# Kernel optimization log

Hardware: AMD Instinct MI355X
Metric: run time of the kernel (lower is better)

The kernel has to match this reference:

```python
import jax, jax.numpy as jnp
import numpy as np

N, E, B = 4096, 4096, 128  # nodes, edges, graphs


def _param(key, shape, scale):
    return jax.random.normal(key, shape, dtype=jnp.float32) * scale


def setup_inputs() -> dict:
    key = jax.random.key(0)
    ks = jax.random.split(key, 32)
    inp = {
        "x": jax.random.normal(ks[0], (N, 37), dtype=jnp.float32),
        "edge_index": jax.random.randint(ks[1], (2, E), 0, N),
        "edge_attr": jax.random.uniform(ks[2], (E, 5), dtype=jnp.float32),
        "batch": jnp.sort(jax.random.randint(ks[3], (N,), 0, B)),
        # NNConv 1: edge-MLP 5->512->37*128, root [37,128]
        "nn1_w1": _param(ks[4], (5, 512), 0.3),
        "nn1_b1": jnp.zeros((512,), jnp.float32),
        "nn1_w2": _param(ks[5], (512, 37 * 128), 0.01),
        "nn1_b2": jnp.zeros((37 * 128,), jnp.float32),
        "root1": _param(ks[6], (37, 128), 0.1),
        "bias1": jnp.zeros((128,), jnp.float32),
        # NNConv 2: edge-MLP 5->128->128*256, root [128,256]
        "nn2_w1": _param(ks[7], (5, 128), 0.3),
        "nn2_b1": jnp.zeros((128,), jnp.float32),
        "nn2_w2": _param(ks[8], (128, 128 * 256), 0.005),
        "nn2_b2": jnp.zeros((128 * 256,), jnp.float32),
        "root2": _param(ks[9], (128, 256), 0.05),
        "bias2": jnp.zeros((256,), jnp.float32),
        # NNConv 3: edge-MLP 5->128->256*256, root [256,256]
        "nn3_w1": _param(ks[10], (5, 128), 0.3),
        "nn3_b1": jnp.zeros((128,), jnp.float32),
        "nn3_w2": _param(ks[11], (128, 256 * 256), 0.005),
        "nn3_b2": jnp.zeros((256 * 256,), jnp.float32),
        "root3": _param(ks[12], (256, 256), 0.05),
        "bias3": jnp.zeros((256,), jnp.float32),
        # readout MLP
        "fc1_w": _param(ks[13], (256, 128), 0.06),
        "fc1_b": jnp.zeros((128,), jnp.float32),
        "fc2_w": _param(ks[14], (128, 64), 0.09),
        "fc2_b": jnp.zeros((64,), jnp.float32),
        "fc3_w": _param(ks[15], (64, 1), 0.12),
        "fc3_b": jnp.zeros((1,), jnp.float32),
    }
    return inp


def _nnconv(x, src, dst, edge_attr, w1, b1, w2, b2, root, bias, cin, cout):
    # edge MLP -> per-edge weight matrix [E, cin, cout]
    h = jax.nn.relu(edge_attr @ w1 + b1)
    W = (h @ w2 + b2).reshape(-1, cin, cout)
    # gather source features, per-edge matvec, scatter-add to targets
    msg = jnp.einsum('ei,eio->eo', x[src], W)          # [E, cout]
    agg = jax.ops.segment_sum(msg, dst, num_segments=x.shape[0])
    return agg + x @ root + bias


def _segment_mean(x, seg, num_segments):
    s = jax.ops.segment_sum(x, seg, num_segments=num_segments)
    cnt = jax.ops.segment_sum(jnp.ones((x.shape[0],), x.dtype), seg,
                              num_segments=num_segments)
    return s / jnp.maximum(cnt, 1.0)[:, None]


def reference(x, edge_index, edge_attr, batch,
              nn1_w1, nn1_b1, nn1_w2, nn1_b2, root1, bias1,
              nn2_w1, nn2_b1, nn2_w2, nn2_b2, root2, bias2,
              nn3_w1, nn3_b1, nn3_w2, nn3_b2, root3, bias3,
              fc1_w, fc1_b, fc2_w, fc2_b, fc3_w, fc3_b):
    src, dst = edge_index[0], edge_index[1]
    h = jax.nn.elu(_nnconv(x, src, dst, edge_attr, nn1_w1, nn1_b1, nn1_w2,
                           nn1_b2, root1, bias1, 37, 128))
    h = jax.nn.elu(_nnconv(h, src, dst, edge_attr, nn2_w1, nn2_b1, nn2_w2,
                           nn2_b2, root2, bias2, 128, 256))
    h = jax.nn.elu(_nnconv(h, src, dst, edge_attr, nn3_w1, nn3_b1, nn3_w2,
                           nn3_b2, root3, bias3, 256, 256))
    g = _segment_mean(h, batch, B)                     # [B, 256]
    g = jax.nn.elu(g @ fc1_w + fc1_b)
    g = jax.nn.elu(g @ fc2_w + fc2_b)
    g = g @ fc3_w + fc3_b
    return g.reshape(-1)
```

## Files before the change

kernel.cpp:

```cpp
#include <hip/hip_runtime.h>
#include <cstdint>
#include <cstddef>

typedef float f32x4 __attribute__((ext_vector_type(4)));
typedef _Float16 f16x8 __attribute__((ext_vector_type(8)));
typedef _Float16 f16x4 __attribute__((ext_vector_type(4)));

__device__ __forceinline__ float elu_f(float x) { return x > 0.f ? x : expm1f(x); }

__device__ __forceinline__ void gload_lds16(const void* g, void* l)
{
    __builtin_amdgcn_global_load_lds(
        (const __attribute__((address_space(1))) void*)g,
        (__attribute__((address_space(3))) void*)l,
        16, 0, 0);
}

__global__ __launch_bounds__(256)
void edge_mlp_kernel(const float* __restrict__ ea,
                     const int* __restrict__ dst, int* __restrict__ cnt,
                     const float* __restrict__ w1a, const float* __restrict__ b1a, _Float16* __restrict__ h1T,
                     const float* __restrict__ w1b, const float* __restrict__ b1b, _Float16* __restrict__ h2T,
                     const float* __restrict__ w1c, const float* __restrict__ b1c, _Float16* __restrict__ h3T,
                     int E)
{
    const int e0  = blockIdx.x * 64;
    const int tid = threadIdx.x;
    const int el  = tid & 63;
    const int cg  = tid >> 6;
    if (tid < 64) atomicAdd(&cnt[dst[e0 + tid]], 1);
    __shared__ float a[64][5];
    for (int i = tid; i < 320; i += 256) a[i / 5][i % 5] = ea[e0 * 5 + i];
    __syncthreads();
    float av[5];
    #pragma unroll
    for (int j = 0; j < 5; ++j) av[j] = a[el][j];

    #pragma unroll 4
    for (int t = 0; t < 128; ++t) {
        const int ch = t * 4 + cg;
        float s = b1a[ch];
        #pragma unroll
        for (int j = 0; j < 5; ++j) s = fmaf(av[j], w1a[j * 512 + ch], s);
        h1T[(size_t)ch * E + e0 + el] = (_Float16)fmaxf(s, 0.f);
    }
    #pragma unroll 4
    for (int t = 0; t < 32; ++t) {
        const int ch = t * 4 + cg;
        float s = b1b[ch];
        float u = b1c[ch];
        #pragma unroll
        for (int j = 0; j < 5; ++j) {
            s = fmaf(av[j], w1b[j * 128 + ch], s);
            u = fmaf(av[j], w1c[j * 128 + ch], u);
        }
        h2T[(size_t)ch * E + e0 + el] = (_Float16)fmaxf(s, 0.f);
        h3T[(size_t)ch * E + e0 + el] = (_Float16)fmaxf(u, 0.f);
    }
}

template <int CIN, int COUT, int KFTOT>
__global__ __launch_bounds__(256)
void pack_w2_kernel(const float* __restrict__ w2, const float* __restrict__ b2,
                    _Float16* __restrict__ w2h, int KH)
{
    __shared__ float tile[32][COUT + 2];
    const int bid = blockIdx.x;
    const int kh  = bid / KFTOT;
    const int c   = bid - kh * KFTOT;
    const int tid = threadIdx.x;
    const int CP  = 32 * COUT;
    for (int i = tid; i < CP; i += 256) {
        int kk = i / COUT, n = i - kk * COUT;
        int kg = c * 32 + kk;
        float v = 0.f;
        if (kg < CIN) v = (kh < KH) ? w2[((size_t)kh * CIN + kg) * COUT + n]
                                    : b2[(size_t)kg * COUT + n];
        tile[kk][n] = v;
    }
    __syncthreads();
    _Float16* outp = w2h + (size_t)bid * CP;
    for (int i = tid; i < CP; i += 256) {
        int n = i >> 5, kk = i & 31;
        int blk = (kk >> 3) ^ ((n >> 1) & 3);
        outp[n * 32 + blk * 8 + (kk & 7)] = (_Float16)tile[kk][n];
    }
}

__global__ __launch_bounds__(256)
void csr_scan_graph_kernel(const int* __restrict__ cnt, int* __restrict__ offs, int N,
                           const int* __restrict__ batch, int* __restrict__ goffs, int B,
                           int NN)
{
    __shared__ int sums[256];
    __shared__ int pref[257];
    const int tid = threadIdx.x;
    const int per = N / 256;
    int loc = 0;
    for (int i = 0; i < per; ++i) loc += cnt[tid * per + i];
    sums[tid] = loc;
    __syncthreads();
    if (tid == 0) {
        int s = 0; pref[0] = 0;
        for (int i = 0; i < 256; ++i) { s += sums[i]; pref[i + 1] = s; }
    }
    __syncthreads();
    int run = pref[tid];
    for (int i = 0; i < per; ++i) { offs[tid * per + i] = run; run += cnt[tid * per + i]; }
    if (tid == 255) offs[N] = run;
    for (int g = tid; g <= B; g += 256) {
        int lo = 0, hi = NN;
        while (lo < hi) { int mid = (lo + hi) >> 1; if (batch[mid] < g) lo = mid + 1; else hi = mid; }
        goffs[g] = lo;
    }
}

__global__ __launch_bounds__(256)
void csr_fill_kernel(const int* __restrict__ dst, const int* __restrict__ offs,
                     int* __restrict__ cur, int* __restrict__ eid, int E)
{
    int e = blockIdx.x * 256 + threadIdx.x;
    if (e < E) {
        int d = dst[e];
        int p = offs[d] + atomicAdd(&cur[d], 1);
        eid[p] = e;
    }
}

template <int KH, int CIN, int COUT, int KFTOT, int CSPLIT, int NY>
__global__ __launch_bounds__(256, 4)
void msg_mfma_kernel(const float* __restrict__ xin,
                     const _Float16* __restrict__ hT,
                     const _Float16* __restrict__ w2h,
                     const int* __restrict__ src,
                     _Float16* __restrict__ part,
                     int E, int khg_per)
{
    constexpr int BM = 128;
    constexpr int KF = KFTOT / CSPLIT;

    __shared__ __align__(16) _Float16 bsh[2][KF][64][32];
    __shared__ _Float16 s_h[2][BM];
    __shared__ int s_src[BM];

    const int tid  = threadIdx.x;
    const int lane = tid & 63;
    const int w    = tid >> 6;
    const int l15  = lane & 15;
    const int lg   = lane >> 4;
    const int swb  = (l15 >> 1) & 3;

    const int nwg = gridDim.x;
    const int bid = blockIdx.x;
    const int swz = (bid & 7) * (nwg >> 3) + (bid >> 3);
    const int m    = swz & 31;
    const int rest = swz >> 5;
    const int y    = rest % NY;
    const int zz   = rest / NY;
    const int cinH = zz % CSPLIT;
    const int zkh  = zz / CSPLIT;

    const int e0  = m * BM;
    const int n0  = y * 64;
    const int k0  = cinH * KF * 32;
    const int kh0 = zkh * khg_per;
    const int kh1 = min(kh0 + khg_per, KH + 1);

    if (tid < BM) s_src[tid] = src[e0 + tid];
    __syncthreads();

    f16x8 a_[2][KF];
    #pragma unroll
    for (int mf = 0; mf < 2; ++mf) {
        const int eloc = w * 32 + mf * 16 + l15;
        const float* xrow = xin + (size_t)s_src[eloc] * CIN + k0;
        #pragma unroll
        for (int c = 0; c < KF; ++c) {
            if (CIN % 32 == 0) {
                float4 p0 = *(const float4*)(xrow + c * 32 + lg * 8);
                float4 p1 = *(const float4*)(xrow + c * 32 + lg * 8 + 4);
                a_[mf][c][0] = (_Float16)p0.x; a_[mf][c][1] = (_Float16)p0.y;
                a_[mf][c][2] = (_Float16)p0.z; a_[mf][c][3] = (_Float16)p0.w;
                a_[mf][c][4] = (_Float16)p1.x; a_[mf][c][5] = (_Float16)p1.y;
                a_[mf][c][6] = (_Float16)p1.z; a_[mf][c][7] = (_Float16)p1.w;
            } else {
                #pragma unroll
                for (int j = 0; j < 8; ++j) {
                    int kk = c * 32 + lg * 8 + j;
                    float v = (k0 + kk < CIN) ? xrow[kk] : 0.f;
                    a_[mf][c][j] = (_Float16)v;
                }
            }
        }
    }

    f32x4 msg[2][4];
    #pragma unroll
    for (int mf = 0; mf < 2; ++mf)
        #pragma unroll
        for (int nf = 0; nf < 4; ++nf) msg[mf][nf] = 0.f;

    auto stage = [&](int khg, int pp) {
        if (khg >= kh1) return;
        const size_t chunk0 = (size_t)khg * KFTOT + cinH * KF;
        const char* g = (const char*)(w2h + (chunk0 * COUT + n0) * 32) + (size_t)tid * 16;
        char* l = (char*)(&bsh[pp][0][0][0]) + (tid >> 6) * 1024;
        #pragma unroll
        for (int c = 0; c < KF; ++c)
            gload_lds16(g + (size_t)c * COUT * 64, l + c * 4096);
    };
    auto stage_h = [&](int khg) {
        if (tid < BM && khg < kh1 && khg < KH)
            s_h[khg & 1][tid] = hT[(size_t)khg * E + e0 + tid];
    };

    int p = 0;
    stage(kh0, 0);
    stage_h(kh0);

    for (int khg = kh0; khg < kh1; ++khg) {
        __syncthreads();

        stage(khg + 1, p ^ 1);
        stage_h(khg + 1);

        _Float16 hh[2];
        #pragma unroll
        for (int mf = 0; mf < 2; ++mf)
            hh[mf] = (khg < KH) ? s_h[khg & 1][w * 32 + mf * 16 + l15] : (_Float16)1.0f;

        #pragma unroll
        for (int c = 0; c < KF; ++c) {
            f16x8 Bv[4];
            #pragma unroll
            for (int nf = 0; nf < 4; ++nf)
                Bv[nf] = *(const f16x8*)&bsh[p][c][nf * 16 + l15][(lg ^ swb) * 8];
            #pragma unroll
            for (int mf = 0; mf < 2; ++mf) {
                f16x8 ah = a_[mf][c] * hh[mf];
                #pragma unroll
                for (int nf = 0; nf < 4; ++nf)
                    msg[mf][nf] = __builtin_amdgcn_mfma_f32_16x16x32_f16(ah, Bv[nf], msg[mf][nf], 0, 0, 0);
            }
        }
        p ^= 1;
    }

    _Float16* pb = part + ((size_t)zz * E + e0) * COUT + n0;
    #pragma unroll
    for (int mf = 0; mf < 2; ++mf)
        #pragma unroll
        for (int r = 0; r < 4; ++r) {
            const int row = w * 32 + mf * 16 + lg * 4 + r;
            #pragma unroll
            for (int nf = 0; nf < 4; ++nf)
                pb[(size_t)row * COUT + nf * 16 + l15] = (_Float16)msg[mf][nf][r];
        }
}

template <int CIN, int COUT, int Z>
__global__ __launch_bounds__(256)
void node_gemm_kernel(const float* __restrict__ xin,
                      const float* __restrict__ root,
                      const _Float16* __restrict__ part,
                      const int* __restrict__ offs,
                      const int* __restrict__ eid,
                      const float* __restrict__ bias,
                      float* __restrict__ out, int E)
{
    constexpr int BM  = 64;
    constexpr int BN  = 64;
    constexpr int BKI = (CIN % 32 == 0) ? 32 : 16;
    constexpr int CIN_PAD = ((CIN + BKI - 1) / BKI) * BKI;
    constexpr int CPK = CIN_PAD / BKI;
    constexpr int NROWS = BKI / 16;

    __shared__ __align__(16) float xs_t[CIN_PAD][BM];
    __shared__ __align__(16) float btile[BKI][BN];

    const int tid = threadIdx.x;
    const int tx  = tid & 15;
    const int ty  = tid >> 4;
    const int ty4 = ty * 4;
    const int tx4 = tx * 4;
    const int e0  = blockIdx.x * BM;
    const int n0  = blockIdx.y * BN;

    for (int idx = tid; idx < BM * CIN_PAD; idx += 256) {
        int mm = idx / CIN_PAD;
        int i  = idx - mm * CIN_PAD;
        float v = 0.f;
        if (i < CIN) v = xin[(size_t)(e0 + mm) * CIN + i];
        xs_t[i][mm] = v;
    }

    const int rbase = tid >> 4;
    const int nn    = (tid & 15) * 4;
    float acc[4][4] = {};
    float4 pre[NROWS];

    {
        const float* brow = root + n0;
        #pragma unroll
        for (int rr = 0; rr < NROWS; ++rr) {
            int r = rbase + rr * 16;
            float4 v = {0.f, 0.f, 0.f, 0.f};
            if (r < CIN) v = *(const float4*)(brow + (size_t)r * COUT + nn);
            pre[rr] = v;
        }
    }

    for (int c = 0; c < CPK; ++c) {
        __syncthreads();
        #pragma unroll
        for (int rr = 0; rr < NROWS; ++rr)
            *(float4*)&btile[rbase + rr * 16][nn] = pre[rr];
        __syncthreads();

        if (c + 1 < CPK) {
            int i0n = (c + 1) * BKI;
            const float* brow = root + (size_t)i0n * COUT + n0;
            #pragma unroll
            for (int rr = 0; rr < NROWS; ++rr) {
                int r = rbase + rr * 16;
                float4 v = {0.f, 0.f, 0.f, 0.f};
                if (i0n + r < CIN) v = *(const float4*)(brow + (size_t)r * COUT + nn);
                pre[rr] = v;
            }
        }

        const int i0 = c * BKI;
        #pragma unroll
        for (int ii = 0; ii < BKI; ++ii) {
            float4 xv = *(const float4*)&xs_t[i0 + ii][ty4];
            float4 bv = *(const float4*)&btile[ii][tx4];
            float av[4] = {xv.x, xv.y, xv.z, xv.w};
            float bvv[4] = {bv.x, bv.y, bv.z, bv.w};
            #pragma unroll
            for (int mm = 0; mm < 4; ++mm)
                #pragma unroll
                for (int nq = 0; nq < 4; ++nq)
                    acc[mm][nq] = fmaf(av[mm], bvv[nq], acc[mm][nq]);
        }
    }

    float bs[4];
    #pragma unroll
    for (int nq = 0; nq < 4; ++nq) bs[nq] = bias[n0 + tx4 + nq];

    #pragma unroll
    for (int mm = 0; mm < 4; ++mm) {
        const int row = e0 + ty4 + mm;
        float add[4] = {0.f, 0.f, 0.f, 0.f};
        const int b = offs[row], t = offs[row + 1];
        for (int j = b; j < t; ++j) {
            const int e = eid[j];
            #pragma unroll
            for (int z = 0; z < Z; ++z) {
                f16x4 r4 = *(const f16x4*)(part + ((size_t)z * E + e) * COUT + n0 + tx4);
                add[0] += (float)r4.x; add[1] += (float)r4.y;
                add[2] += (float)r4.z; add[3] += (float)r4.w;
            }
        }
        size_t base = (size_t)row * COUT + n0 + tx4;
        #pragma unroll
        for (int nq = 0; nq < 4; ++nq)
            out[base + nq] = elu_f(acc[mm][nq] + add[nq] + bs[nq]);
    }
}

__global__ __launch_bounds__(256)
void pool_readout_kernel(const float* __restrict__ hl3, const int* __restrict__ goffs,
                         const float* __restrict__ fc1w, const float* __restrict__ fc1b,
                         const float* __restrict__ fc2w, const float* __restrict__ fc2b,
                         const float* __restrict__ fc3w, const float* __restrict__ fc3b,
                         float* __restrict__ outp)
{
    const int g   = blockIdx.x;
    const int tid = threadIdx.x;
    __shared__ float gm[256];
    __shared__ float a1[128];
    __shared__ float a2[64];
    const int b = goffs[g], t = goffs[g + 1];
    float s = 0.f;
    for (int n = b; n < t; ++n) s += hl3[(size_t)n * 256 + tid];
    gm[tid] = s / fmaxf((float)(t - b), 1.f);
    __syncthreads();
    if (tid < 128) {
        float v = fc1b[tid];
        for (int j = 0; j < 256; ++j) v = fmaf(gm[j], fc1w[j * 128 + tid], v);
        a1[tid] = elu_f(v);
    }
    __syncthreads();
    if (tid < 64) {
        float v = fc2b[tid];
        for (int j = 0; j < 128; ++j) v = fmaf(a1[j], fc2w[j * 64 + tid], v);
        a2[tid] = elu_f(v);
    }
    __syncthreads();
    if (tid == 0) {
        float v = fc3b[0];
        for (int j = 0; j < 64; ++j) v = fmaf(a2[j], fc3w[j], v);
        outp[g] = v;
    }
}

extern "C" void kernel_launch(void* const* d_in, const int* in_sizes, int n_in,
                              void* d_out, int out_size, void* d_ws, size_t ws_size,
                              hipStream_t stream)
{
    const float* x      = (const float*)d_in[0];
    const int*   ei     = (const int*)  d_in[1];
    const float* ea     = (const float*)d_in[2];
    const int*   batch  = (const int*)  d_in[3];
    const float* nn1_w1 = (const float*)d_in[4];
    const float* nn1_b1 = (const float*)d_in[5];
    const float* nn1_w2 = (const float*)d_in[6];
    const float* nn1_b2 = (const float*)d_in[7];
    const float* root1  = (const float*)d_in[8];
    const float* bias1  = (const float*)d_in[9];
    const float* nn2_w1 = (const float*)d_in[10];
    const float* nn2_b1 = (const float*)d_in[11];
    const float* nn2_w2 = (const float*)d_in[12];
    const float* nn2_b2 = (const float*)d_in[13];
    const float* root2  = (const float*)d_in[14];
    const float* bias2  = (const float*)d_in[15];
    const float* nn3_w1 = (const float*)d_in[16];
    const float* nn3_b1 = (const float*)d_in[17];
    const float* nn3_w2 = (const float*)d_in[18];
    const float* nn3_b2 = (const float*)d_in[19];
    const float* root3  = (const float*)d_in[20];
    const float* bias3  = (const float*)d_in[21];
    const float* fc1_w  = (const float*)d_in[22];
    const float* fc1_b  = (const float*)d_in[23];
    const float* fc2_w  = (const float*)d_in[24];
    const float* fc2_b  = (const float*)d_in[25];
    const float* fc3_w  = (const float*)d_in[26];
    const float* fc3_b  = (const float*)d_in[27];

    const int E = in_sizes[2] / 5;
    const int N = in_sizes[0] / 37;
    const int B = out_size;
    const int* srcp = ei;
    const int* dstp = ei + E;

    const size_t W1H = (size_t)513 * 2 * 128 * 32;
    const size_t W2H = (size_t)129 * 4 * 256 * 32;
    const size_t W3H = (size_t)129 * 8 * 256 * 32;
    _Float16* w2h1 = (_Float16*)d_ws;
    _Float16* w2h2 = w2h1 + W1H;
    _Float16* w2h3 = w2h2 + W2H;
    _Float16* h1T  = w2h3 + W3H;
    _Float16* h2T  = h1T + (size_t)512 * E;
    _Float16* h3T  = h2T + (size_t)128 * E;
    _Float16* part = h3T + (size_t)128 * E;
    float* fbase = (float*)(part + (size_t)16 * E * 128);
    float* hl1   = fbase;
    float* hl2   = hl1 + (size_t)N * 128;
    float* hl3   = hl2 + (size_t)N * 256;
    int* ibase   = (int*)(hl3 + (size_t)N * 256);
    int* cnt   = ibase;
    int* cur   = cnt + N;
    int* offs  = cur + N;
    int* eid   = offs + N + 1;
    int* goffs = eid + E;

    hipMemsetAsync(cnt, 0, 2 * N * sizeof(int), stream);

    edge_mlp_kernel<<<E / 64, 256, 0, stream>>>(ea, dstp, cnt,
                                                nn1_w1, nn1_b1, h1T,
                                                nn2_w1, nn2_b1, h2T,
                                                nn3_w1, nn3_b1, h3T, E);

    pack_w2_kernel<37, 128, 2><<<513 * 2, 256, 0, stream>>>(nn1_w2, nn1_b2, w2h1, 512);
    pack_w2_kernel<128, 256, 4><<<129 * 4, 256, 0, stream>>>(nn2_w2, nn2_b2, w2h2, 128);
    pack_w2_kernel<256, 256, 8><<<129 * 8, 256, 0, stream>>>(nn3_w2, nn3_b2, w2h3, 128);

    csr_scan_graph_kernel<<<1, 256, 0, stream>>>(cnt, offs, N, batch, goffs, B, N);
    csr_fill_kernel<<<(E + 255) / 256, 256, 0, stream>>>(dstp, offs, cur, eid, E);

    msg_mfma_kernel<512, 37, 128, 2, 1, 2><<<1024, 256, 0, stream>>>(
        x, h1T, w2h1, srcp, part, E, 33);
    node_gemm_kernel<37, 128, 16><<<dim3(N / 64, 2), 256, 0, stream>>>(
        x, root1, part, offs, eid, bias1, hl1, E);

    msg_mfma_kernel<128, 128, 256, 4, 1, 4><<<1024, 256, 0, stream>>>(
        hl1, h2T, w2h2, srcp, part, E, 17);
    node_gemm_kernel<128, 256, 8><<<dim3(N / 64, 4), 256, 0, stream>>>(
        hl1, root2, part, offs, eid, bias2, hl2, E);

    msg_mfma_kernel<128, 256, 256, 8, 2, 4><<<1024, 256, 0, stream>>>(
        hl2, h3T, w2h3, srcp, part, E, 33);
    node_gemm_kernel<256, 256, 8><<<dim3(N / 64, 4), 256, 0, stream>>>(
        hl2, root3, part, offs, eid, bias3, hl3, E);

    pool_readout_kernel<<<B, 256, 0, stream>>>(hl3, goffs, fc1_w, fc1_b,
                                               fc2_w, fc2_b, fc3_w, fc3_b,
                                               (float*)d_out);
}
```

Measured before the change: 312.4 us.

## Fuse prologue kernels and double message-tile rows with wider channel/K splits

Merges the edge-MLP and the three weight-packing kernels into one launch that dispatches on block index. It also doubles the message GEMM M tile from 128 to 256 edges per block, which gives more MFMA reuse of each staged weight tile. To keep the grid at 1024 blocks it increases the input-channel or K-group splits, so more fp16 partial buffers (Z doubled) must be written and then reduced in node_gemm. The trade-off is higher register pressure from the 4x4 accumulators, plus more partial-sum traffic.

```diff
diff --git a/kernel.cpp b/kernel.cpp
--- a/kernel.cpp
+++ b/kernel.cpp
@@ -16,75 +16,87 @@
         16, 0, 0);
 }
 
-__global__ __launch_bounds__(256)
-void edge_mlp_kernel(const float* __restrict__ ea,
-                     const int* __restrict__ dst, int* __restrict__ cnt,
-                     const float* __restrict__ w1a, const float* __restrict__ b1a, _Float16* __restrict__ h1T,
-                     const float* __restrict__ w1b, const float* __restrict__ b1b, _Float16* __restrict__ h2T,
-                     const float* __restrict__ w1c, const float* __restrict__ b1c, _Float16* __restrict__ h3T,
-                     int E)
-{
-    const int e0  = blockIdx.x * 64;
-    const int tid = threadIdx.x;
-    const int el  = tid & 63;
-    const int cg  = tid >> 6;
-    if (tid < 64) atomicAdd(&cnt[dst[e0 + tid]], 1);
-    __shared__ float a[64][5];
-    for (int i = tid; i < 320; i += 256) a[i / 5][i % 5] = ea[e0 * 5 + i];
-    __syncthreads();
-    float av[5];
-    #pragma unroll
-    for (int j = 0; j < 5; ++j) av[j] = a[el][j];
-
-    #pragma unroll 4
-    for (int t = 0; t < 128; ++t) {
-        const int ch = t * 4 + cg;
-        float s = b1a[ch];
-        #pragma unroll
-        for (int j = 0; j < 5; ++j) s = fmaf(av[j], w1a[j * 512 + ch], s);
-        h1T[(size_t)ch * E + e0 + el] = (_Float16)fmaxf(s, 0.f);
-    }
-    #pragma unroll 4
-    for (int t = 0; t < 32; ++t) {
-        const int ch = t * 4 + cg;
-        float s = b1b[ch];
-        float u = b1c[ch];
-        #pragma unroll
-        for (int j = 0; j < 5; ++j) {
-            s = fmaf(av[j], w1b[j * 128 + ch], s);
-            u = fmaf(av[j], w1c[j * 128 + ch], u);
-        }
-        h2T[(size_t)ch * E + e0 + el] = (_Float16)fmaxf(s, 0.f);
-        h3T[(size_t)ch * E + e0 + el] = (_Float16)fmaxf(u, 0.f);
-    }
-}
-
 template <int CIN, int COUT, int KFTOT>
-__global__ __launch_bounds__(256)
-void pack_w2_kernel(const float* __restrict__ w2, const float* __restrict__ b2,
-                    _Float16* __restrict__ w2h, int KH)
-{
-    __shared__ float tile[32][COUT + 2];
-    const int bid = blockIdx.x;
-    const int kh  = bid / KFTOT;
-    const int c   = bid - kh * KFTOT;
-    const int tid = threadIdx.x;
-    const int CP  = 32 * COUT;
+__device__ __forceinline__
+void pack_body(int bid, int tid, const float* __restrict__ w2, const float* __restrict__ b2,
+               _Float16* __restrict__ w2h, int KH, float* tile )
+{
+    const int kh = bid / KFTOT;
+    const int c  = bid - kh * KFTOT;
+    const int CP = 32 * COUT;
     for (int i = tid; i < CP; i += 256) {
         int kk = i / COUT, n = i - kk * COUT;
         int kg = c * 32 + kk;
         float v = 0.f;
         if (kg < CIN) v = (kh < KH) ? w2[((size_t)kh * CIN + kg) * COUT + n]
                                     : b2[(size_t)kg * COUT + n];
-        tile[kk][n] = v;
+        tile[kk * (COUT + 2) + n] = v;
     }
     __syncthreads();
     _Float16* outp = w2h + (size_t)bid * CP;
     for (int i = tid; i < CP; i += 256) {
         int n = i >> 5, kk = i & 31;
         int blk = (kk >> 3) ^ ((n >> 1) & 3);
-        outp[n * 32 + blk * 8 + (kk & 7)] = (_Float16)tile[kk][n];
-    }
+        outp[n * 32 + blk * 8 + (kk & 7)] = (_Float16)tile[kk * (COUT + 2) + n];
+    }
+}
+
+__global__ __launch_bounds__(256)
+void uber_prologue_kernel(const float* __restrict__ ea,
+                          const int* __restrict__ dst, int* __restrict__ cnt,
+                          const float* __restrict__ w1a, const float* __restrict__ b1a, _Float16* __restrict__ h1T,
+                          const float* __restrict__ w1b, const float* __restrict__ b1b, _Float16* __restrict__ h2T,
+                          const float* __restrict__ w1c, const float* __restrict__ b1c, _Float16* __restrict__ h3T,
+                          int E,
+                          const float* __restrict__ w2a, const float* __restrict__ b2a, _Float16* __restrict__ w2h1,
+                          const float* __restrict__ w2b, const float* __restrict__ b2b, _Float16* __restrict__ w2h2,
+                          const float* __restrict__ w2c, const float* __restrict__ b2c, _Float16* __restrict__ w2h3)
+{
+    __shared__ __align__(16) float smem[32 * 258];
+    const int tid = threadIdx.x;
+    const int nEB = E >> 6;
+    int b = blockIdx.x;
+
+    if (b < nEB) {
+        const int e0 = b * 64;
+        const int el = tid & 63;
+        const int cg = tid >> 6;
+        if (tid < 64) atomicAdd(&cnt[dst[e0 + tid]], 1);
+        float* a = smem;
+        for (int i = tid; i < 320; i += 256) a[(i / 5) * 5 + (i % 5)] = ea[e0 * 5 + i];
+        __syncthreads();
+        float av[5];
+        #pragma unroll
+        for (int j = 0; j < 5; ++j) av[j] = a[el * 5 + j];
+        #pragma unroll 4
+        for (int t = 0; t < 128; ++t) {
+            const int ch = t * 4 + cg;
+            float s = b1a[ch];
+            #pragma unroll
+            for (int j = 0; j < 5; ++j) s = fmaf(av[j], w1a[j * 512 + ch], s);
+            h1T[(size_t)ch * E + e0 + el] = (_Float16)fmaxf(s, 0.f);
+        }
+        #pragma unroll 4
+        for (int t = 0; t < 32; ++t) {
+            const int ch = t * 4 + cg;
+            float s = b1b[ch];
+            float u = b1c[ch];
+            #pragma unroll
+            for (int j = 0; j < 5; ++j) {
+                s = fmaf(av[j], w1b[j * 128 + ch], s);
+                u = fmaf(av[j], w1c[j * 128 + ch], u);
+            }
+            h2T[(size_t)ch * E + e0 + el] = (_Float16)fmaxf(s, 0.f);
+            h3T[(size_t)ch * E + e0 + el] = (_Float16)fmaxf(u, 0.f);
+        }
+        return;
+    }
+    b -= nEB;
+    if (b < 513 * 2) { pack_body<37, 128, 2>(b, tid, w2a, b2a, w2h1, 512, smem); return; }
+    b -= 513 * 2;
+    if (b < 129 * 4) { pack_body<128, 256, 4>(b, tid, w2b, b2b, w2h2, 128, smem); return; }
+    b -= 129 * 4;
+    pack_body<256, 256, 8>(b, tid, w2c, b2c, w2h3, 128, smem);
 }
 
 __global__ __launch_bounds__(256)
@@ -136,7 +148,7 @@
                      _Float16* __restrict__ part,
                      int E, int khg_per)
 {
-    constexpr int BM = 128;
+    constexpr int BM = 256;
     constexpr int KF = KFTOT / CSPLIT;
 
     __shared__ __align__(16) _Float16 bsh[2][KF][64][32];
@@ -153,8 +165,8 @@
     const int nwg = gridDim.x;
     const int bid = blockIdx.x;
     const int swz = (bid & 7) * (nwg >> 3) + (bid >> 3);
-    const int m    = swz & 31;
-    const int rest = swz >> 5;
+    const int m    = swz & 15;
+    const int rest = swz >> 4;
     const int y    = rest % NY;
     const int zz   = rest / NY;
     const int cinH = zz % CSPLIT;
@@ -166,13 +178,13 @@
     const int kh0 = zkh * khg_per;
     const int kh1 = min(kh0 + khg_per, KH + 1);
 
-    if (tid < BM) s_src[tid] = src[e0 + tid];
-    __syncthreads();
-
-    f16x8 a_[2][KF];
+    s_src[tid] = src[e0 + tid];
+    __syncthreads();
+
+    f16x8 a_[4][KF];
     #pragma unroll
-    for (int mf = 0; mf < 2; ++mf) {
-        const int eloc = w * 32 + mf * 16 + l15;
+    for (int mf = 0; mf < 4; ++mf) {
+        const int eloc = w * 64 + mf * 16 + l15;
         const float* xrow = xin + (size_t)s_src[eloc] * CIN + k0;
         #pragma unroll
         for (int c = 0; c < KF; ++c) {
@@ -194,9 +206,9 @@
         }
     }
 
-    f32x4 msg[2][4];
+    f32x4 msg[4][4];
     #pragma unroll
-    for (int mf = 0; mf < 2; ++mf)
+    for (int mf = 0; mf < 4; ++mf)
         #pragma unroll
         for (int nf = 0; nf < 4; ++nf) msg[mf][nf] = 0.f;
 
@@ -210,8 +222,7 @@
             gload_lds16(g + (size_t)c * COUT * 64, l + c * 4096);
     };
     auto stage_h = [&](int khg) {
-        if (tid < BM && khg < kh1 && khg < KH)
-            s_h[khg & 1][tid] = hT[(size_t)khg * E + e0 + tid];
+        if (khg < kh1 && khg < KH) s_h[khg & 1][tid] = hT[(size_t)khg * E + e0 + tid];
     };
 
     int p = 0;
@@ -224,10 +235,10 @@
         stage(khg + 1, p ^ 1);
         stage_h(khg + 1);
 
-        _Float16 hh[2];
-        #pragma unroll
-        for (int mf = 0; mf < 2; ++mf)
-            hh[mf] = (khg < KH) ? s_h[khg & 1][w * 32 + mf * 16 + l15] : (_Float16)1.0f;
+        _Float16 hh[4];
+        #pragma unroll
+        for (int mf = 0; mf < 4; ++mf)
+            hh[mf] = (khg < KH) ? s_h[khg & 1][w * 64 + mf * 16 + l15] : (_Float16)1.0f;
 
         #pragma unroll
         for (int c = 0; c < KF; ++c) {
@@ -236,7 +247,7 @@
             for (int nf = 0; nf < 4; ++nf)
                 Bv[nf] = *(const f16x8*)&bsh[p][c][nf * 16 + l15][(lg ^ swb) * 8];
             #pragma unroll
-            for (int mf = 0; mf < 2; ++mf) {
+            for (int mf = 0; mf < 4; ++mf) {
                 f16x8 ah = a_[mf][c] * hh[mf];
                 #pragma unroll
                 for (int nf = 0; nf < 4; ++nf)
@@ -248,10 +259,10 @@
 
     _Float16* pb = part + ((size_t)zz * E + e0) * COUT + n0;
     #pragma unroll
-    for (int mf = 0; mf < 2; ++mf)
+    for (int mf = 0; mf < 4; ++mf)
         #pragma unroll
         for (int r = 0; r < 4; ++r) {
-            const int row = w * 32 + mf * 16 + lg * 4 + r;
+            const int row = w * 64 + mf * 16 + lg * 4 + r;
             #pragma unroll
             for (int nf = 0; nf < 4; ++nf)
                 pb[(size_t)row * COUT + nf * 16 + l15] = (_Float16)msg[mf][nf][r];
@@ -454,7 +465,7 @@
     _Float16* h2T  = h1T + (size_t)512 * E;
     _Float16* h3T  = h2T + (size_t)128 * E;
     _Float16* part = h3T + (size_t)128 * E;
-    float* fbase = (float*)(part + (size_t)16 * E * 128);
+    float* fbase = (float*)(part + (size_t)32 * E * 128);
     float* hl1   = fbase;
     float* hl2   = hl1 + (size_t)N * 128;
     float* hl3   = hl2 + (size_t)N * 256;
@@ -467,31 +478,28 @@
 
     hipMemsetAsync(cnt, 0, 2 * N * sizeof(int), stream);
 
-    edge_mlp_kernel<<<E / 64, 256, 0, stream>>>(ea, dstp, cnt,
-                                                nn1_w1, nn1_b1, h1T,
-                                                nn2_w1, nn2_b1, h2T,
-                                                nn3_w1, nn3_b1, h3T, E);
-
-    pack_w2_kernel<37, 128, 2><<<513 * 2, 256, 0, stream>>>(nn1_w2, nn1_b2, w2h1, 512);
-    pack_w2_kernel<128, 256, 4><<<129 * 4, 256, 0, stream>>>(nn2_w2, nn2_b2, w2h2, 128);
-    pack_w2_kernel<256, 256, 8><<<129 * 8, 256, 0, stream>>>(nn3_w2, nn3_b2, w2h3, 128);
+    const int nEB = E / 64;
+    uber_prologue_kernel<<<nEB + 1026 + 516 + 1032, 256, 0, stream>>>(
+        ea, dstp, cnt,
+        nn1_w1, nn1_b1, h1T, nn2_w1, nn2_b1, h2T, nn3_w1, nn3_b1, h3T, E,
+        nn1_w2, nn1_b2, w2h1, nn2_w2, nn2_b2, w2h2, nn3_w2, nn3_b2, w2h3);
 
     csr_scan_graph_kernel<<<1, 256, 0, stream>>>(cnt, offs, N, batch, goffs, B, N);
     csr_fill_kernel<<<(E + 255) / 256, 256, 0, stream>>>(dstp, offs, cur, eid, E);
 
     msg_mfma_kernel<512, 37, 128, 2, 1, 2><<<1024, 256, 0, stream>>>(
-        x, h1T, w2h1, srcp, part, E, 33);
-    node_gemm_kernel<37, 128, 16><<<dim3(N / 64, 2), 256, 0, stream>>>(
+        x, h1T, w2h1, srcp, part, E, 17);
+    node_gemm_kernel<37, 128, 32><<<dim3(N / 64, 2), 256, 0, stream>>>(
         x, root1, part, offs, eid, bias1, hl1, E);
 
-    msg_mfma_kernel<128, 128, 256, 4, 1, 4><<<1024, 256, 0, stream>>>(
+    msg_mfma_kernel<128, 128, 256, 4, 2, 4><<<1024, 256, 0, stream>>>(
         hl1, h2T, w2h2, srcp, part, E, 17);
-    node_gemm_kernel<128, 256, 8><<<dim3(N / 64, 4), 256, 0, stream>>>(
+    node_gemm_kernel<128, 256, 16><<<dim3(N / 64, 4), 256, 0, stream>>>(
         hl1, root2, part, offs, eid, bias2, hl2, E);
 
-    msg_mfma_kernel<128, 256, 256, 8, 2, 4><<<1024, 256, 0, stream>>>(
+    msg_mfma_kernel<128, 256, 256, 8, 4, 4><<<1024, 256, 0, stream>>>(
         hl2, h3T, w2h3, srcp, part, E, 33);
-    node_gemm_kernel<256, 256, 8><<<dim3(N / 64, 4), 256, 0, stream>>>(
+    node_gemm_kernel<256, 256, 16><<<dim3(N / 64, 4), 256, 0, stream>>>(
         hl2, root3, part, offs, eid, bias3, hl3, E);
 
     pool_readout_kernel<<<B, 256, 0, stream>>>(hl3, goffs, fc1_w, fc1_b,
```

Result: faster. 292.1 us (-6.5%).
